# Optimization experiments

Measured on AMD Instinct MI355X. Metric: run time of the kernel, lower is better.

Reference implementation:

```python
import jax, jax.numpy as jnp
import numpy as np

B, S, D_H, D_L, K, K_H, W = 4, 4096, 1024, 256, 64, 4, 9


def setup_inputs() -> dict:
    key = jax.random.key(0)
    ks = jax.random.split(key, 6)
    return {
        "inputs": jax.random.normal(ks[0], (B, S, D_H), jnp.float32),
        "W1": jax.random.normal(ks[1], (D_H, D_L), jnp.float32) * 0.02,
        "b1": jnp.zeros((D_L,), jnp.float32),
        "RME": jax.random.normal(ks[2], (D_L, K), jnp.float32),
        "K2": jax.random.normal(ks[3], (K_H, D_L, D_L), jnp.float32) * 0.02,
        "b2": jnp.zeros((D_L,), jnp.float32),
        "Wu": jax.random.normal(ks[4], (D_L, D_H), jnp.float32) * 0.02,
        "bu": jnp.zeros((D_H,), jnp.float32),
        "gamma": jnp.ones((D_H,), jnp.float32),
        "beta": jnp.zeros((D_H,), jnp.float32),
    }


def _memory_reorg(act, RMVs, k_h):
    # act: [B,S,d_l], RMVs: [B,S,k]
    R = jnp.transpose(RMVs, (0, 2, 1))  # [B,k,S]
    h_vars = jnp.mean((R - jnp.mean(R, axis=-1, keepdims=True)) ** 2, axis=-1)  # [B,k]
    top = jnp.argsort(-h_vars, axis=-1)[:, :k_h]                   # [B,k_h]
    h_max = jnp.take_along_axis(R, top[:, :, None], axis=1)        # [B,k_h,S]
    perm = jnp.argsort(h_max, axis=-1)                             # [B,k_h,S] permutation indices
    g = jnp.take_along_axis(act[:, None], perm[..., None], axis=2) # [B,k_h,S,d_l]
    return jnp.transpose(g, (0, 2, 1, 3))                          # [B,S,k_h,d_l]


def reference(inputs, W1, b1, RME, K2, b2, Wu, bu, gamma, beta):
    # DOWN_PROJECTION_1
    q = jax.nn.relu(jnp.einsum('bsh,hd->bsd', inputs, W1) + b1)    # [B,S,d_l]
    # RANDOM_PROJECTION
    RMVs = jnp.einsum('bsd,dk->bsk', q, RME)                       # [B,S,k]
    # Memory reorganization (variance-based argsort permutations)
    qp = _memory_reorg(q, RMVs, K_H)                               # [B,S,k_h,d_l]
    # DOWN_PROJECTION_2
    q2 = jax.nn.relu(jnp.einsum('bskd,kde->bse', qp, K2) + b2)     # [B,S,d_l]
    # Sliding-window key construction (edge windows replicated)
    half = (W - 1) // 2
    widx = jnp.arange(S - W + 1)[:, None] + jnp.arange(W)[None, :]  # [S-W+1, W]
    win = q2[:, widx]                                               # [B,S-W+1,W,d_l]
    first = jnp.broadcast_to(q2[:, None, :W], (B, half, W, D_L))
    last = jnp.broadcast_to(q2[:, None, S - W:], (B, half, W, D_L))
    keyt = jnp.concatenate([first, win, last], axis=1)              # [B,S,W,d_l]
    # Windowed attention
    f = jnp.sqrt(jnp.float32(D_L))
    scores = jax.nn.softmax(jnp.einsum('bsd,bswd->bsw', q2, keyt) / f, axis=-1)  # [B,S,W]
    # UP_PROJECTION on keys -> values
    val = jax.nn.relu(jnp.einsum('bswd,dh->bswh', keyt, Wu) + bu)   # [B,S,W,d_h]
    out = jnp.einsum('bswh,bsw->bsh', val, scores)                  # [B,S,d_h]
    # LayerNorm (keras default epsilon=1e-3) on residual
    x = out + inputs
    mu = jnp.mean(x, axis=-1, keepdims=True)
    var = jnp.mean((x - mu) ** 2, axis=-1, keepdims=True)
    return gamma * (x - mu) * jax.lax.rsqrt(var + 1e-3) + beta
```

## Files before the change

### kernel.cpp

```cpp
#include <hip/hip_runtime.h>

#define B_  4
#define S_  4096
#define DH  1024
#define DL  256
#define KK  64
#define KH  4
#define WW  9

typedef unsigned short ushort_t;
typedef _Float16 f16;
typedef _Float16 f16x8 __attribute__((ext_vector_type(8)));
typedef float  f32x4  __attribute__((ext_vector_type(4)));

__device__ __forceinline__ void gld_lds16(const void* g, void* lds_uniform_base) {
    __builtin_amdgcn_global_load_lds(
        (const __attribute__((address_space(1))) unsigned int*)g,
        (__attribute__((address_space(3))) unsigned int*)lds_uniform_base,
        16, 0, 0);
}

template<bool AFP32, bool GATHER, bool WL>
__global__ __launch_bounds__(256)
void mfma_gemm_sm(const float* __restrict__ Af,
                  const ushort_t* __restrict__ Ah, const ushort_t* __restrict__ Al,
                  const ushort_t* __restrict__ Bh, const ushort_t* __restrict__ Bl,
                  const float* __restrict__ bias, float* __restrict__ C,
                  ushort_t* __restrict__ Ch, ushort_t* __restrict__ Cl,
                  const int* __restrict__ gidx, int K, int N, int nbx)
{
    __shared__ __align__(16) ushort_t Abuf[64 * 64 * 2];
    __shared__ __align__(16) ushort_t Bsh[64 * 64];
    __shared__ __align__(16) ushort_t Bsl[64 * 64];

    const int tid = threadIdx.x;
    const int w = tid >> 6, l = tid & 63;
    const int wm = w >> 1, wn = w & 1;
    const int lr = l & 15, lk = l >> 4;
    const int cpx = gridDim.x >> 3;
    const int orig = (blockIdx.x & 7) * cpx + (blockIdx.x >> 3);
    const int m0 = (orig / nbx) * 64, n0 = (orig % nbx) * 64;

    f32x4 acc0[2][2] = {};
    f32x4 acc1[2][2] = {};

    for (int k0 = 0; k0 < K; k0 += 64) {
        if (AFP32) {
            float* Asf = (float*)Abuf;
            #pragma unroll
            for (int it = 0; it < 4; ++it) {
                const int c = it * 256 + tid;
                const int r = c >> 4, cc = c & 15;
                const int cs = cc ^ ((r & 7) << 1);
                const float* src = Af + (size_t)(m0 + r) * K + k0 + cs * 4;
                gld_lds16(src, &Asf[(size_t)c * 4]);
            }
        } else {
            ushort_t* Ash = Abuf;
            ushort_t* Asl = Abuf + 64 * 64;
            #pragma unroll
            for (int it = 0; it < 2; ++it) {
                const int c = it * 256 + tid;
                const int r = c >> 3, kp = c & 7;
                const int kl = kp ^ (r & 7);
                size_t offA;
                if (GATHER) {
                    const int rg = gidx[(m0 + r) * KH + (k0 >> 8)];
                    offA = (size_t)rg * DL + (k0 & (DL - 1)) + kl * 8;
                } else {
                    offA = (size_t)(m0 + r) * K + k0 + kl * 8;
                }
                gld_lds16(Ah + offA, &Ash[(size_t)c * 8]);
                gld_lds16(Al + offA, &Asl[(size_t)c * 8]);
            }
        }
        #pragma unroll
        for (int it = 0; it < 2; ++it) {
            const int c = it * 256 + tid;
            const int r = c >> 3, kp = c & 7;
            const int kl = kp ^ (r & 7);
            const size_t off = (size_t)(n0 + r) * K + k0 + kl * 8;
            gld_lds16(Bh + off, &Bsh[(size_t)c * 8]);
            gld_lds16(Bl + off, &Bsl[(size_t)c * 8]);
        }
        __syncthreads();

        #pragma unroll
        for (int ks = 0; ks < 2; ++ks) {
            f16x8 ah[2], al[2];
            #pragma unroll
            for (int mf = 0; mf < 2; ++mf) {
                const int row = wm * 32 + mf * 16 + lr;
                const int kb  = ks * 4 + lk;
                if (AFP32) {
                    const float* Asf = (const float*)Abuf;
                    const int fo = row * 64 + ((kb ^ (row & 7)) << 3);
                    const f32x4 lo = *(const f32x4*)&Asf[fo];
                    const f32x4 hi = *(const f32x4*)&Asf[fo + 4];
                    const float xs[8] = {lo[0], lo[1], lo[2], lo[3],
                                         hi[0], hi[1], hi[2], hi[3]};
                    #pragma unroll
                    for (int e = 0; e < 8; ++e) {
                        const f16 h = (f16)xs[e];
                        const f16 lv = (f16)((xs[e] - (float)h) * 2048.0f);
                        ah[mf][e] = h;
                        al[mf][e] = lv;
                    }
                } else {
                    const ushort_t* Ash = Abuf;
                    const ushort_t* Asl = Abuf + 64 * 64;
                    const int o = row * 64 + ((kb ^ (row & 7)) << 3);
                    ah[mf] = *(const f16x8*)&Ash[o];
                    al[mf] = *(const f16x8*)&Asl[o];
                }
            }
            #pragma unroll
            for (int nf = 0; nf < 2; ++nf) {
                const int row = wn * 32 + nf * 16 + lr;
                const int kb  = ks * 4 + lk;
                const int o   = row * 64 + ((kb ^ (row & 7)) << 3);
                const f16x8 bh = *(const f16x8*)&Bsh[o];
                const f16x8 bl = *(const f16x8*)&Bsl[o];
                #pragma unroll
                for (int mf = 0; mf < 2; ++mf) {
                    acc0[mf][nf] = __builtin_amdgcn_mfma_f32_16x16x32_f16(
                        ah[mf], bh, acc0[mf][nf], 0, 0, 0);
                    acc1[mf][nf] = __builtin_amdgcn_mfma_f32_16x16x32_f16(
                        ah[mf], bl, acc1[mf][nf], 0, 0, 0);
                    acc1[mf][nf] = __builtin_amdgcn_mfma_f32_16x16x32_f16(
                        al[mf], bh, acc1[mf][nf], 0, 0, 0);
                }
            }
        }
        __syncthreads();
    }

    float bv[2];
    #pragma unroll
    for (int nf = 0; nf < 2; ++nf)
        bv[nf] = bias[n0 + wn * 32 + nf * 16 + lr];
    #pragma unroll
    for (int mf = 0; mf < 2; ++mf)
        #pragma unroll
        for (int nf = 0; nf < 2; ++nf)
            #pragma unroll
            for (int r = 0; r < 4; ++r) {
                const int m = m0 + wm * 32 + mf * 16 + lk * 4 + r;
                const int n = n0 + wn * 32 + nf * 16 + lr;
                float x = acc0[mf][nf][r] + acc1[mf][nf][r] * (1.0f / 2048.0f) + bv[nf];
                x = fmaxf(x, 0.f);
                C[(size_t)m * N + n] = x;
                const f16 h = (f16)x;
                Ch[(size_t)m * N + n] = __builtin_bit_cast(ushort_t, h);
                if (WL) {
                    const f16 lo = (f16)((x - (float)h) * 2048.0f);
                    Cl[(size_t)m * N + n] = __builtin_bit_cast(ushort_t, lo);
                }
            }
}

__global__ __launch_bounds__(512)
void mfma_gemm1l(const ushort_t* __restrict__ Ah, const ushort_t* __restrict__ Bh,
                 const float* __restrict__ bias, ushort_t* __restrict__ Ch,
                 int K, int N, int nbx)
{
    __shared__ __align__(16) ushort_t Ash[128 * 64];
    __shared__ __align__(16) ushort_t Bsh[128 * 64];

    const int tid = threadIdx.x;
    const int w = tid >> 6, l = tid & 63;
    const int wm = w >> 1, wn = w & 1;
    const int lr = l & 15, lk = l >> 4;
    const int cpx = gridDim.x >> 3;
    const int orig = (blockIdx.x & 7) * cpx + (blockIdx.x >> 3);
    const int m0 = (orig / nbx) * 128, n0 = (orig % nbx) * 128;

    f32x4 acc0[2][4] = {};

    for (int k0 = 0; k0 < K; k0 += 64) {
        #pragma unroll
        for (int it = 0; it < 2; ++it) {
            const int c = it * 512 + tid;
            const int r = c >> 3, kp = c & 7;
            const int kl = kp ^ (r & 7);
            const size_t offA = (size_t)(m0 + r) * K + k0 + kl * 8;
            const size_t offB = (size_t)(n0 + r) * K + k0 + kl * 8;
            gld_lds16(Ah + offA, &Ash[(size_t)c * 8]);
            gld_lds16(Bh + offB, &Bsh[(size_t)c * 8]);
        }
        __syncthreads();

        #pragma unroll
        for (int ks = 0; ks < 2; ++ks) {
            f16x8 ah[2];
            #pragma unroll
            for (int mf = 0; mf < 2; ++mf) {
                const int row = wm * 32 + mf * 16 + lr;
                const int kb  = ks * 4 + lk;
                ah[mf] = *(const f16x8*)&Ash[row * 64 + ((kb ^ (row & 7)) << 3)];
            }
            #pragma unroll
            for (int nf = 0; nf < 4; ++nf) {
                const int row = wn * 64 + nf * 16 + lr;
                const int kb  = ks * 4 + lk;
                const f16x8 bh = *(const f16x8*)&Bsh[row * 64 + ((kb ^ (row & 7)) << 3)];
                #pragma unroll
                for (int mf = 0; mf < 2; ++mf)
                    acc0[mf][nf] = __builtin_amdgcn_mfma_f32_16x16x32_f16(
                        ah[mf], bh, acc0[mf][nf], 0, 0, 0);
            }
        }
        __syncthreads();
    }

    float bv[4];
    #pragma unroll
    for (int nf = 0; nf < 4; ++nf)
        bv[nf] = bias[n0 + wn * 64 + nf * 16 + lr];
    #pragma unroll
    for (int mf = 0; mf < 2; ++mf)
        #pragma unroll
        for (int nf = 0; nf < 4; ++nf)
            #pragma unroll
            for (int r = 0; r < 4; ++r) {
                const int m = m0 + wm * 32 + mf * 16 + lk * 4 + r;
                const int n = n0 + wn * 64 + nf * 16 + lr;
                float x = acc0[mf][nf][r] + bv[nf];
                x = fmaxf(x, 0.f);
                const f16 hcv = (f16)x;
                Ch[(size_t)m * N + n] = __builtin_bit_cast(ushort_t, hcv);
            }
}

__global__ __launch_bounds__(256)
void tsplit2_kernel(const float* __restrict__ in, ushort_t* __restrict__ t0,
                    ushort_t* __restrict__ t1, int K, int N)
{
    __shared__ float tile[32][33];
    const int t = threadIdx.x;
    const int bk = blockIdx.x * 32, bn = blockIdx.y * 32;
    const int c = t & 31, rb = t >> 5;
    #pragma unroll
    for (int i = 0; i < 4; ++i) {
        const int r = rb + i * 8;
        tile[r][c] = in[(size_t)(bk + r) * N + bn + c];
    }
    __syncthreads();
    #pragma unroll
    for (int i = 0; i < 4; ++i) {
        const int rr = rb + i * 8;
        const float x = tile[c][rr];
        const f16 hv = (f16)x;
        const f16 lv = (f16)((x - (float)hv) * 2048.0f);
        const size_t o = (size_t)(bn + rr) * K + bk + c;
        t0[o] = __builtin_bit_cast(ushort_t, hv);
        t1[o] = __builtin_bit_cast(ushort_t, lv);
    }
}

__global__ __launch_bounds__(256)
void gemm_trans_kernel(const float* __restrict__ A, const float* __restrict__ Bm,
                       float* __restrict__ C, int M, int KA, int N)
{
    constexpr int BK = 16;
    __shared__ float Asb[BK][64 + 4];
    __shared__ float Bsb[BK][64 + 4];
    const int tid = threadIdx.x;
    const int tx = tid & 15, ty = tid >> 4;
    const int m0 = blockIdx.y * 64, n0 = blockIdx.x * 64;

    float acc[4][4] = {};
    const int lr = tid >> 2, lc = (tid & 3) << 2;
    const int kr = tid >> 4, nc = (tid & 15) << 2;

    for (int k0 = 0; k0 < KA; k0 += BK) {
        const float4 a4 = *reinterpret_cast<const float4*>(A + (size_t)(m0 + lr) * KA + k0 + lc);
        const float4 b4 = *reinterpret_cast<const float4*>(Bm + (size_t)(k0 + kr) * N + n0 + nc);
        Asb[lc + 0][lr] = a4.x; Asb[lc + 1][lr] = a4.y;
        Asb[lc + 2][lr] = a4.z; Asb[lc + 3][lr] = a4.w;
        *reinterpret_cast<float4*>(&Bsb[kr][nc]) = b4;
        __syncthreads();
        #pragma unroll
        for (int kk = 0; kk < BK; ++kk) {
            const float4 av = *reinterpret_cast<const float4*>(&Asb[kk][ty << 2]);
            const float4 bv = *reinterpret_cast<const float4*>(&Bsb[kk][tx << 2]);
            const float a[4] = {av.x, av.y, av.z, av.w};
            const float b[4] = {bv.x, bv.y, bv.z, bv.w};
            #pragma unroll
            for (int i = 0; i < 4; ++i)
                #pragma unroll
                for (int j = 0; j < 4; ++j)
                    acc[i][j] = fmaf(a[i], b[j], acc[i][j]);
        }
        __syncthreads();
    }
    #pragma unroll
    for (int i = 0; i < 4; ++i) {
        const int m = m0 + (ty << 2) + i;
        const int b = m >> 12, s = m & (S_ - 1);
        #pragma unroll
        for (int j = 0; j < 4; ++j) {
            const int n = n0 + (tx << 2) + j;
            C[(size_t)(b * N + n) * S_ + s] = acc[i][j];
        }
    }
}

__global__ __launch_bounds__(256)
void var_kernel(const float* __restrict__ rmvT, float* __restrict__ hvars)
{
    const int bk = blockIdx.x;
    const float* src = rmvT + (size_t)bk * S_;
    float s1 = 0.f, s2 = 0.f;
    for (int t = threadIdx.x; t < S_; t += 256) {
        const float v = src[t];
        s1 += v; s2 += v * v;
    }
    #pragma unroll
    for (int off = 32; off; off >>= 1) {
        s1 += __shfl_xor(s1, off);
        s2 += __shfl_xor(s2, off);
    }
    __shared__ float r1[4], r2[4];
    const int wave = threadIdx.x >> 6, lane = threadIdx.x & 63;
    if (lane == 0) { r1[wave] = s1; r2[wave] = s2; }
    __syncthreads();
    if (threadIdx.x == 0) {
        const float t1 = r1[0] + r1[1] + r1[2] + r1[3];
        const float t2 = r2[0] + r2[1] + r2[2] + r2[3];
        const float mu = t1 / (float)S_;
        hvars[bk] = t2 / (float)S_ - mu * mu;
    }
}

__global__ void topk_kernel(const float* __restrict__ hvars, int* __restrict__ topidx)
{
    const int b = threadIdx.x;
    if (b >= B_) return;
    float v[KK];
    for (int k = 0; k < KK; ++k) v[k] = hvars[b * KK + k];
    for (int i = 0; i < KH; ++i) {
        int best = 0; float bv = -3.4e38f;
        for (int k = 0; k < KK; ++k)
            if (v[k] > bv) { bv = v[k]; best = k; }
        topidx[b * KH + i] = best;
        v[best] = -3.4e38f;
    }
}

__global__ __launch_bounds__(256)
void rank_kernel(const float* __restrict__ rmvT, const int* __restrict__ topidx,
                 int* __restrict__ gidx)
{
    const int bi = blockIdx.x;
    const int b = bi >> 2, ih = bi & 3;
    const int k = topidx[b * KH + ih];
    const float* src = rmvT + (size_t)(b * KK + k) * S_;
    __shared__ __align__(16) unsigned long long keys[S_];
    __shared__ int partial[4][64];
    for (int t = threadIdx.x; t < S_; t += 256) {
        const unsigned bits = __builtin_bit_cast(unsigned, src[t]);
        const unsigned u = (bits & 0x80000000u) ? ~bits : (bits | 0x80000000u);
        keys[t] = ((unsigned long long)u << 12) | (unsigned)t;
    }
    __syncthreads();

    const int il = threadIdx.x & 63;
    const int chunk = threadIdx.x >> 6;
    const int i = blockIdx.y * 64 + il;
    const unsigned long long ki = keys[i];

    int cnt = 0;
    const int jbase = chunk << 10;
    #pragma unroll 8
    for (int jj = 0; jj < 1024; jj += 2) {
        const ulonglong2 k2 = *reinterpret_cast<const ulonglong2*>(&keys[jbase + jj]);
        cnt += (int)(k2.x < ki);
        cnt += (int)(k2.y < ki);
    }
    partial[chunk][il] = cnt;
    __syncthreads();
    if (threadIdx.x < 64) {
        const int rank = partial[0][threadIdx.x] + partial[1][threadIdx.x]
                       + partial[2][threadIdx.x] + partial[3][threadIdx.x];
        const int ii = blockIdx.y * 64 + threadIdx.x;
        gidx[((b << 12) + rank) * KH + ih] = (b << 12) + ii;
    }
}

__global__ __launch_bounds__(256)
void final_kernel(const ushort_t* __restrict__ vh, const float* __restrict__ q2,
                  const float* __restrict__ inputs, const float* __restrict__ gamma,
                  const float* __restrict__ beta, float* __restrict__ out)
{
    const int bid = blockIdx.x;
    const int m0 = (((bid & 7) << 9) | (bid >> 3)) << 2;
    const int wave = threadIdx.x >> 6, lane = threadIdx.x & 63;
    const int m = m0 + wave;
    const int s = m & (S_ - 1), b = m >> 12;
    const int jb = (s < 4) ? 0 : (s >= S_ - 4 ? S_ - WW : s - 4);

    const ushort_t* vb = vh + (size_t)(b * S_ + jb) * DH;
    const float* inp = inputs + (size_t)m * DH;
    f16x8 varr[2][WW];
    float4 iv[2][2];
    #pragma unroll
    for (int c = 0; c < 2; ++c) {
        const int h = (c << 9) + (lane << 3);
        #pragma unroll
        for (int w = 0; w < WW; ++w)
            varr[c][w] = *reinterpret_cast<const f16x8*>(vb + (size_t)w * DH + h);
        iv[c][0] = *reinterpret_cast<const float4*>(inp + h);
        iv[c][1] = *reinterpret_cast<const float4*>(inp + h + 4);
    }

    const float4 qv = *reinterpret_cast<const float4*>(q2 + (size_t)m * DL + (lane << 2));
    const float* kbase = q2 + (size_t)(b * S_ + jb) * DL;
    float sc[WW];
    #pragma unroll
    for (int w = 0; w < WW; ++w) {
        const float4 kv = *reinterpret_cast<const float4*>(kbase + w * DL + (lane << 2));
        float d = qv.x * kv.x + qv.y * kv.y + qv.z * kv.z + qv.w * kv.w;
        #pragma unroll
        for (int off = 32; off; off >>= 1) d += __shfl_xor(d, off);
        sc[w] = d * 0.0625f;
    }
    float mx = sc[0];
    #pragma unroll
    for (int w = 1; w < WW; ++w) mx = fmaxf(mx, sc[w]);
    float wgt[WW]; float sum = 0.f;
    #pragma unroll
    for (int w = 0; w < WW; ++w) { wgt[w] = __expf(sc[w] - mx); sum += wgt[w]; }
    const float inv = 1.f / sum;
    #pragma unroll
    for (int w = 0; w < WW; ++w) wgt[w] *= inv;

    float x[2][8];
    float s1 = 0.f, s2 = 0.f;
    #pragma unroll
    for (int c = 0; c < 2; ++c) {
        float acc[8] = {};
        #pragma unroll
        for (int w = 0; w < WW; ++w) {
            const f16x8 vv = varr[c][w];
            #pragma unroll
            for (int e = 0; e < 8; ++e)
                acc[e] = fmaf(wgt[w], (float)vv[e], acc[e]);
        }
        #pragma unroll
        for (int e = 0; e < 8; ++e) {
            const float ivv = (e < 4) ? (&iv[c][0].x)[e] : (&iv[c][1].x)[e - 4];
            acc[e] += ivv;
            x[c][e] = acc[e];
            s1 += acc[e];
            s2 += acc[e] * acc[e];
        }
    }

    #pragma unroll
    for (int off = 32; off; off >>= 1) {
        s1 += __shfl_xor(s1, off);
        s2 += __shfl_xor(s2, off);
    }
    const float mu = s1 / (float)DH;
    const float rs = rsqrtf(s2 / (float)DH - mu * mu + 0.001f);

    #pragma unroll
    for (int c = 0; c < 2; ++c) {
        const int h = (c << 9) + (lane << 3);
        #pragma unroll
        for (int half = 0; half < 2; ++half) {
            const float4 g  = *reinterpret_cast<const float4*>(gamma + h + half * 4);
            const float4 bt = *reinterpret_cast<const float4*>(beta + h + half * 4);
            float4 o;
            o.x = g.x * (x[c][half * 4 + 0] - mu) * rs + bt.x;
            o.y = g.y * (x[c][half * 4 + 1] - mu) * rs + bt.y;
            o.z = g.z * (x[c][half * 4 + 2] - mu) * rs + bt.z;
            o.w = g.w * (x[c][half * 4 + 3] - mu) * rs + bt.w;
            *reinterpret_cast<float4*>(out + (size_t)m * DH + h + half * 4) = o;
        }
    }
}

extern "C" void kernel_launch(void* const* d_in, const int* in_sizes, int n_in,
                              void* d_out, int out_size, void* d_ws, size_t ws_size,
                              hipStream_t stream)
{
    (void)in_sizes; (void)n_in; (void)out_size; (void)ws_size;
    const float* inputs = (const float*)d_in[0];
    const float* W1     = (const float*)d_in[1];
    const float* b1     = (const float*)d_in[2];
    const float* RME    = (const float*)d_in[3];
    const float* K2     = (const float*)d_in[4];
    const float* b2     = (const float*)d_in[5];
    const float* Wu     = (const float*)d_in[6];
    const float* bu     = (const float*)d_in[7];
    const float* gamma  = (const float*)d_in[8];
    const float* beta   = (const float*)d_in[9];
    float* out = (float*)d_out;

    char* ws = (char*)d_ws;
    const size_t MB = 1u << 20;
    ushort_t* vh  = (ushort_t*)(ws + 0 * MB);
    float*    q   = (float*)   (ws + 64 * MB);
    ushort_t* qh  = (ushort_t*)(ws + 80 * MB);
    ushort_t* ql  = (ushort_t*)(ws + 88 * MB);
    float*    q2  = (float*)   (ws + 96 * MB);
    ushort_t* q2h = (ushort_t*)(ws + 112 * MB);
    float*    rmvT= (float*)   (ws + 128 * MB);
    float*    hvars  = (float*)(ws + 132 * MB);
    int*      topidx = (int*)  (ws + 132 * MB + 4096);
    int*      gidx   = (int*)  (ws + 132 * MB + 8192);
    ushort_t* w1th = (ushort_t*)(ws + 133 * MB);
    ushort_t* w1tl = w1th + (DH * DL);
    ushort_t* k2th = w1tl + (DH * DL);
    ushort_t* k2tl = k2th + (KH * DL * DL);
    ushort_t* wuth = k2tl + (KH * DL * DL);
    ushort_t* wutl = wuth + (DL * DH);

    const int M = B_ * S_;

    tsplit2_kernel<<<dim3(DH / 32, DL / 32), dim3(256), 0, stream>>>(W1, w1th, w1tl, DH, DL);
    tsplit2_kernel<<<dim3(KH * DL / 32, DL / 32), dim3(256), 0, stream>>>((const float*)K2, k2th, k2tl, KH * DL, DL);
    tsplit2_kernel<<<dim3(DL / 32, DH / 32), dim3(256), 0, stream>>>(Wu, wuth, wutl, DL, DH);

    mfma_gemm_sm<true, false, true><<<dim3((DL / 64) * (M / 64)), dim3(256), 0, stream>>>(
        inputs, nullptr, nullptr, w1th, w1tl, b1, q, qh, ql, nullptr, DH, DL, DL / 64);
    gemm_trans_kernel<<<dim3(KK / 64, M / 64), dim3(256), 0, stream>>>(q, RME, rmvT, M, DL, KK);
    var_kernel<<<dim3(B_ * KK), dim3(256), 0, stream>>>(rmvT, hvars);
    topk_kernel<<<dim3(1), dim3(64), 0, stream>>>(hvars, topidx);
    rank_kernel<<<dim3(B_ * KH, S_ / 64), dim3(256), 0, stream>>>(rmvT, topidx, gidx);
    mfma_gemm_sm<false, true, false><<<dim3((DL / 64) * (M / 64)), dim3(256), 0, stream>>>(
        nullptr, qh, ql, k2th, k2tl, b2, q2, q2h, nullptr, gidx, KH * DL, DL, DL / 64);
    mfma_gemm1l<<<dim3((DH / 128) * (M / 128)), dim3(512), 0, stream>>>(
        q2h, wuth, bu, vh, DL, DH, DH / 128);
    final_kernel<<<dim3(M / 4), dim3(256), 0, stream>>>(vh, q2, inputs, gamma, beta, out);
}
```

Before: 189.2 us.

## Double-buffer LDS staging in MFMA GEMMs and use fp16 q2 in final kernel

Both MFMA GEMM kernels now double-buffer their LDS tiles, issuing global-to-LDS loads for the next K slice before computing the current one, so memory latency can overlap compute. The gather indices for the K2 GEMM are preloaded into registers once rather than reloaded every K step. The fp32 q2 output is dropped; the final attention kernel reads the fp16 copy instead, which halves that traffic but lowers score precision. Doubled LDS use may reduce occupancy, and there is a possible race because the next stage's async loads are not waited on before the barrier.

```diff
diff --git a/kernel.cpp b/kernel.cpp
--- a/kernel.cpp
+++ b/kernel.cpp
@@ -20,7 +20,7 @@
         16, 0, 0);
 }
 
-template<bool AFP32, bool GATHER, bool WL>
+template<bool AFP32, bool GATHER, int OUTMODE>
 __global__ __launch_bounds__(256)
 void mfma_gemm_sm(const float* __restrict__ Af,
                   const ushort_t* __restrict__ Ah, const ushort_t* __restrict__ Al,
@@ -29,9 +29,8 @@
                   ushort_t* __restrict__ Ch, ushort_t* __restrict__ Cl,
                   const int* __restrict__ gidx, int K, int N, int nbx)
 {
-    __shared__ __align__(16) ushort_t Abuf[64 * 64 * 2];
-    __shared__ __align__(16) ushort_t Bsh[64 * 64];
-    __shared__ __align__(16) ushort_t Bsl[64 * 64];
+    __shared__ __align__(16) ushort_t Abuf[2][64 * 64 * 2];
+    __shared__ __align__(16) ushort_t Bbuf[2][2][64 * 64];
 
     const int tid = threadIdx.x;
     const int w = tid >> 6, l = tid & 63;
@@ -41,23 +40,29 @@
     const int orig = (blockIdx.x & 7) * cpx + (blockIdx.x >> 3);
     const int m0 = (orig / nbx) * 64, n0 = (orig % nbx) * 64;
 
-    f32x4 acc0[2][2] = {};
-    f32x4 acc1[2][2] = {};
-
-    for (int k0 = 0; k0 < K; k0 += 64) {
+    int rg[2][KH];
+    if (GATHER) {
+        const int r0 = tid >> 3;
+        #pragma unroll
+        for (int it = 0; it < 2; ++it)
+            #pragma unroll
+            for (int h = 0; h < KH; ++h)
+                rg[it][h] = gidx[(m0 + it * 32 + r0) * KH + h];
+    }
+
+    auto stage = [&](int buf, int k0) {
         if (AFP32) {
-            float* Asf = (float*)Abuf;
+            float* Asf = (float*)Abuf[buf];
             #pragma unroll
             for (int it = 0; it < 4; ++it) {
                 const int c = it * 256 + tid;
                 const int r = c >> 4, cc = c & 15;
                 const int cs = cc ^ ((r & 7) << 1);
-                const float* src = Af + (size_t)(m0 + r) * K + k0 + cs * 4;
-                gld_lds16(src, &Asf[(size_t)c * 4]);
+                gld_lds16(Af + (size_t)(m0 + r) * K + k0 + cs * 4, &Asf[(size_t)c * 4]);
             }
         } else {
-            ushort_t* Ash = Abuf;
-            ushort_t* Asl = Abuf + 64 * 64;
+            ushort_t* Ash = Abuf[buf];
+            ushort_t* Asl = Abuf[buf] + 64 * 64;
             #pragma unroll
             for (int it = 0; it < 2; ++it) {
                 const int c = it * 256 + tid;
@@ -65,8 +70,7 @@
                 const int kl = kp ^ (r & 7);
                 size_t offA;
                 if (GATHER) {
-                    const int rg = gidx[(m0 + r) * KH + (k0 >> 8)];
-                    offA = (size_t)rg * DL + (k0 & (DL - 1)) + kl * 8;
+                    offA = (size_t)rg[it][k0 >> 8] * DL + (k0 & (DL - 1)) + kl * 8;
                 } else {
                     offA = (size_t)(m0 + r) * K + k0 + kl * 8;
                 }
@@ -80,10 +84,19 @@
             const int r = c >> 3, kp = c & 7;
             const int kl = kp ^ (r & 7);
             const size_t off = (size_t)(n0 + r) * K + k0 + kl * 8;
-            gld_lds16(Bh + off, &Bsh[(size_t)c * 8]);
-            gld_lds16(Bl + off, &Bsl[(size_t)c * 8]);
-        }
-        __syncthreads();
+            gld_lds16(Bh + off, &Bbuf[buf][0][(size_t)c * 8]);
+            gld_lds16(Bl + off, &Bbuf[buf][1][(size_t)c * 8]);
+        }
+    };
+
+    f32x4 acc0[2][2] = {};
+    f32x4 acc1[2][2] = {};
+
+    stage(0, 0);
+    __syncthreads();
+    int cur = 0;
+    for (int k0 = 0; k0 < K; k0 += 64) {
+        if (k0 + 64 < K) stage(cur ^ 1, k0 + 64);
 
         #pragma unroll
         for (int ks = 0; ks < 2; ++ks) {
@@ -93,7 +106,7 @@
                 const int row = wm * 32 + mf * 16 + lr;
                 const int kb  = ks * 4 + lk;
                 if (AFP32) {
-                    const float* Asf = (const float*)Abuf;
+                    const float* Asf = (const float*)Abuf[cur];
                     const int fo = row * 64 + ((kb ^ (row & 7)) << 3);
                     const f32x4 lo = *(const f32x4*)&Asf[fo];
                     const f32x4 hi = *(const f32x4*)&Asf[fo + 4];
@@ -107,8 +120,8 @@
                         al[mf][e] = lv;
                     }
                 } else {
-                    const ushort_t* Ash = Abuf;
-                    const ushort_t* Asl = Abuf + 64 * 64;
+                    const ushort_t* Ash = Abuf[cur];
+                    const ushort_t* Asl = Abuf[cur] + 64 * 64;
                     const int o = row * 64 + ((kb ^ (row & 7)) << 3);
                     ah[mf] = *(const f16x8*)&Ash[o];
                     al[mf] = *(const f16x8*)&Asl[o];
@@ -119,8 +132,8 @@
                 const int row = wn * 32 + nf * 16 + lr;
                 const int kb  = ks * 4 + lk;
                 const int o   = row * 64 + ((kb ^ (row & 7)) << 3);
-                const f16x8 bh = *(const f16x8*)&Bsh[o];
-                const f16x8 bl = *(const f16x8*)&Bsl[o];
+                const f16x8 bh = *(const f16x8*)&Bbuf[cur][0][o];
+                const f16x8 bl = *(const f16x8*)&Bbuf[cur][1][o];
                 #pragma unroll
                 for (int mf = 0; mf < 2; ++mf) {
                     acc0[mf][nf] = __builtin_amdgcn_mfma_f32_16x16x32_f16(
@@ -133,6 +146,7 @@
             }
         }
         __syncthreads();
+        cur ^= 1;
     }
 
     float bv[2];
@@ -149,10 +163,12 @@
                 const int n = n0 + wn * 32 + nf * 16 + lr;
                 float x = acc0[mf][nf][r] + acc1[mf][nf][r] * (1.0f / 2048.0f) + bv[nf];
                 x = fmaxf(x, 0.f);
-                C[(size_t)m * N + n] = x;
                 const f16 h = (f16)x;
-                Ch[(size_t)m * N + n] = __builtin_bit_cast(ushort_t, h);
-                if (WL) {
+                if (OUTMODE == 2) {
+                    Ch[(size_t)m * N + n] = __builtin_bit_cast(ushort_t, h);
+                } else {
+                    C[(size_t)m * N + n] = x;
+                    Ch[(size_t)m * N + n] = __builtin_bit_cast(ushort_t, h);
                     const f16 lo = (f16)((x - (float)h) * 2048.0f);
                     Cl[(size_t)m * N + n] = __builtin_bit_cast(ushort_t, lo);
                 }
@@ -164,8 +180,8 @@
                  const float* __restrict__ bias, ushort_t* __restrict__ Ch,
                  int K, int N, int nbx)
 {
-    __shared__ __align__(16) ushort_t Ash[128 * 64];
-    __shared__ __align__(16) ushort_t Bsh[128 * 64];
+    __shared__ __align__(16) ushort_t Ash[2][128 * 64];
+    __shared__ __align__(16) ushort_t Bsh[2][128 * 64];
 
     const int tid = threadIdx.x;
     const int w = tid >> 6, l = tid & 63;
@@ -175,9 +191,7 @@
     const int orig = (blockIdx.x & 7) * cpx + (blockIdx.x >> 3);
     const int m0 = (orig / nbx) * 128, n0 = (orig % nbx) * 128;
 
-    f32x4 acc0[2][4] = {};
-
-    for (int k0 = 0; k0 < K; k0 += 64) {
+    auto stage = [&](int buf, int k0) {
         #pragma unroll
         for (int it = 0; it < 2; ++it) {
             const int c = it * 512 + tid;
@@ -185,10 +199,18 @@
             const int kl = kp ^ (r & 7);
             const size_t offA = (size_t)(m0 + r) * K + k0 + kl * 8;
             const size_t offB = (size_t)(n0 + r) * K + k0 + kl * 8;
-            gld_lds16(Ah + offA, &Ash[(size_t)c * 8]);
-            gld_lds16(Bh + offB, &Bsh[(size_t)c * 8]);
-        }
-        __syncthreads();
+            gld_lds16(Ah + offA, &Ash[buf][(size_t)c * 8]);
+            gld_lds16(Bh + offB, &Bsh[buf][(size_t)c * 8]);
+        }
+    };
+
+    f32x4 acc0[2][4] = {};
+
+    stage(0, 0);
+    __syncthreads();
+    int cur = 0;
+    for (int k0 = 0; k0 < K; k0 += 64) {
+        if (k0 + 64 < K) stage(cur ^ 1, k0 + 64);
 
         #pragma unroll
         for (int ks = 0; ks < 2; ++ks) {
@@ -197,13 +219,13 @@
             for (int mf = 0; mf < 2; ++mf) {
                 const int row = wm * 32 + mf * 16 + lr;
                 const int kb  = ks * 4 + lk;
-                ah[mf] = *(const f16x8*)&Ash[row * 64 + ((kb ^ (row & 7)) << 3)];
+                ah[mf] = *(const f16x8*)&Ash[cur][row * 64 + ((kb ^ (row & 7)) << 3)];
             }
             #pragma unroll
             for (int nf = 0; nf < 4; ++nf) {
                 const int row = wn * 64 + nf * 16 + lr;
                 const int kb  = ks * 4 + lk;
-                const f16x8 bh = *(const f16x8*)&Bsh[row * 64 + ((kb ^ (row & 7)) << 3)];
+                const f16x8 bh = *(const f16x8*)&Bsh[cur][row * 64 + ((kb ^ (row & 7)) << 3)];
                 #pragma unroll
                 for (int mf = 0; mf < 2; ++mf)
                     acc0[mf][nf] = __builtin_amdgcn_mfma_f32_16x16x32_f16(
@@ -211,6 +233,7 @@
             }
         }
         __syncthreads();
+        cur ^= 1;
     }
 
     float bv[4];
@@ -389,7 +412,7 @@
 }
 
 __global__ __launch_bounds__(256)
-void final_kernel(const ushort_t* __restrict__ vh, const float* __restrict__ q2,
+void final_kernel(const ushort_t* __restrict__ vh, const ushort_t* __restrict__ q2h,
                   const float* __restrict__ inputs, const float* __restrict__ gamma,
                   const float* __restrict__ beta, float* __restrict__ out)
 {
@@ -414,13 +437,20 @@
         iv[c][1] = *reinterpret_cast<const float4*>(inp + h + 4);
     }
 
-    const float4 qv = *reinterpret_cast<const float4*>(q2 + (size_t)m * DL + (lane << 2));
-    const float* kbase = q2 + (size_t)(b * S_ + jb) * DL;
+    const ushort4 qv4 = *reinterpret_cast<const ushort4*>(q2h + (size_t)m * DL + (lane << 2));
+    const float qx = (float)__builtin_bit_cast(f16, qv4.x);
+    const float qy = (float)__builtin_bit_cast(f16, qv4.y);
+    const float qz = (float)__builtin_bit_cast(f16, qv4.z);
+    const float qw = (float)__builtin_bit_cast(f16, qv4.w);
+    const ushort_t* kbase = q2h + (size_t)(b * S_ + jb) * DL;
     float sc[WW];
     #pragma unroll
     for (int w = 0; w < WW; ++w) {
-        const float4 kv = *reinterpret_cast<const float4*>(kbase + w * DL + (lane << 2));
-        float d = qv.x * kv.x + qv.y * kv.y + qv.z * kv.z + qv.w * kv.w;
+        const ushort4 kv4 = *reinterpret_cast<const ushort4*>(kbase + w * DL + (lane << 2));
+        float d = qx * (float)__builtin_bit_cast(f16, kv4.x)
+                + qy * (float)__builtin_bit_cast(f16, kv4.y)
+                + qz * (float)__builtin_bit_cast(f16, kv4.z)
+                + qw * (float)__builtin_bit_cast(f16, kv4.w);
         #pragma unroll
         for (int off = 32; off; off >>= 1) d += __shfl_xor(d, off);
         sc[w] = d * 0.0625f;
@@ -505,7 +535,6 @@
     float*    q   = (float*)   (ws + 64 * MB);
     ushort_t* qh  = (ushort_t*)(ws + 80 * MB);
     ushort_t* ql  = (ushort_t*)(ws + 88 * MB);
-    float*    q2  = (float*)   (ws + 96 * MB);
     ushort_t* q2h = (ushort_t*)(ws + 112 * MB);
     float*    rmvT= (float*)   (ws + 128 * MB);
     float*    hvars  = (float*)(ws + 132 * MB);
@@ -524,15 +553,15 @@
     tsplit2_kernel<<<dim3(KH * DL / 32, DL / 32), dim3(256), 0, stream>>>((const float*)K2, k2th, k2tl, KH * DL, DL);
     tsplit2_kernel<<<dim3(DL / 32, DH / 32), dim3(256), 0, stream>>>(Wu, wuth, wutl, DL, DH);
 
-    mfma_gemm_sm<true, false, true><<<dim3((DL / 64) * (M / 64)), dim3(256), 0, stream>>>(
+    mfma_gemm_sm<true, false, 1><<<dim3((DL / 64) * (M / 64)), dim3(256), 0, stream>>>(
         inputs, nullptr, nullptr, w1th, w1tl, b1, q, qh, ql, nullptr, DH, DL, DL / 64);
     gemm_trans_kernel<<<dim3(KK / 64, M / 64), dim3(256), 0, stream>>>(q, RME, rmvT, M, DL, KK);
     var_kernel<<<dim3(B_ * KK), dim3(256), 0, stream>>>(rmvT, hvars);
     topk_kernel<<<dim3(1), dim3(64), 0, stream>>>(hvars, topidx);
     rank_kernel<<<dim3(B_ * KH, S_ / 64), dim3(256), 0, stream>>>(rmvT, topidx, gidx);
-    mfma_gemm_sm<false, true, false><<<dim3((DL / 64) * (M / 64)), dim3(256), 0, stream>>>(
-        nullptr, qh, ql, k2th, k2tl, b2, q2, q2h, nullptr, gidx, KH * DL, DL, DL / 64);
+    mfma_gemm_sm<false, true, 2><<<dim3((DL / 64) * (M / 64)), dim3(256), 0, stream>>>(
+        nullptr, qh, ql, k2th, k2tl, b2, nullptr, q2h, nullptr, gidx, KH * DL, DL, DL / 64);
     mfma_gemm1l<<<dim3((DH / 128) * (M / 128)), dim3(512), 0, stream>>>(
         q2h, wuth, bu, vh, DL, DH, DH / 128);
-    final_kernel<<<dim3(M / 4), dim3(256), 0, stream>>>(vh, q2, inputs, gamma, beta, out);
-}
+    final_kernel<<<dim3(M / 4), dim3(256), 0, stream>>>(vh, q2h, inputs, gamma, beta, out);
+}
```

New measurement: 195.6 us. +3.4%, slower.
